# Optimization experiments

Hardware: AMD Instinct MI355X
Metric: run time of the kernel (lower is better)

## Reference

```python
import jax, jax.numpy as jnp
import numpy as np

N = 10000    # nodes in batched graph
E = 160000   # edges (avg degree 16)
G = 64       # graphs in batch
F_IN = 128
H = 256      # hidden width (forced equal everywhere by fc_1(1024,..) and readout sums)
HEADS = 2


def setup_inputs() -> dict:
    ks = jax.random.split(jax.random.key(0), 24)
    def w(k, shape, fan_in):
        return jax.random.normal(k, shape, dtype=jnp.float32) * np.float32(1.0 / np.sqrt(fan_in))
    return {
        "h": jax.random.normal(ks[0], (N, F_IN), dtype=jnp.float32),
        "src": jax.random.randint(ks[1], (E,), 0, N, dtype=jnp.int32),
        "dst": jax.random.randint(ks[2], (E,), 0, N, dtype=jnp.int32),
        # sorted graph ids, every graph guaranteed non-empty (avoids -inf from MaxPooling)
        "graph_ids": ((jnp.arange(N) * G) // N).astype(jnp.int32),
        "gcn1_W": w(ks[3], (F_IN, H), F_IN), "gcn1_b": jnp.zeros((H,), jnp.float32),
        "gcn2_W": w(ks[4], (H, H), H),       "gcn2_b": jnp.zeros((H,), jnp.float32),
        "gcn3_W": w(ks[5], (H, H), H),       "gcn3_b": jnp.zeros((H,), jnp.float32),
        "gat1_W": w(ks[6], (F_IN, HEADS * H), F_IN),
        "gat1_al": w(ks[7], (HEADS, H), H), "gat1_ar": w(ks[8], (HEADS, H), H),
        "gat1_b": jnp.zeros((HEADS * H,), jnp.float32),
        "gat2_W": w(ks[9], (H, HEADS * H), H),
        "gat2_al": w(ks[10], (HEADS, H), H), "gat2_ar": w(ks[11], (HEADS, H), H),
        "gat2_b": jnp.zeros((HEADS * H,), jnp.float32),
        "gat3_W": w(ks[12], (H, HEADS * H), H),
        "gat3_al": w(ks[13], (HEADS, H), H), "gat3_ar": w(ks[14], (HEADS, H), H),
        "gat3_b": jnp.zeros((HEADS * H,), jnp.float32),
        "fc1_W": w(ks[15], (4 * H, 128), 4 * H), "fc1_b": jnp.zeros((128,), jnp.float32),
        "fc2_W": w(ks[16], (128, 2), 128),       "fc2_b": jnp.zeros((2,), jnp.float32),
    }


def _forward(h, src, dst, graph_ids,
             gcn1_W, gcn1_b, gcn2_W, gcn2_b, gcn3_W, gcn3_b,
             gat1_W, gat1_al, gat1_ar, gat1_b,
             gat2_W, gat2_al, gat2_ar, gat2_b,
             gat3_W, gat3_al, gat3_ar, gat3_b,
             fc1_W, fc1_b, fc2_W, fc2_b):
    ones_e = jnp.ones((E,), jnp.float32)
    # DGL GraphConv norm='both': D_out^{-1/2} on src side, D_in^{-1/2} on dst side (deg clamped to 1)
    d_src = jnp.clip(jax.ops.segment_sum(ones_e, src, num_segments=N), 1.0) ** -0.5
    d_dst = jnp.clip(jax.ops.segment_sum(ones_e, dst, num_segments=N), 1.0) ** -0.5
    counts = jnp.clip(jax.ops.segment_sum(jnp.ones((N,), jnp.float32), graph_ids, num_segments=G), 1.0)

    def gcn(x, W, b):
        agg = jax.ops.segment_sum((x * d_src[:, None])[src], dst, num_segments=N) * d_dst[:, None]
        return jax.nn.relu(agg @ W + b)

    def gat(x, W, al, ar, b):
        z = (x @ W).reshape(N, HEADS, H)                 # [N, heads, H]
        e = jax.nn.leaky_relu(jnp.sum(z * al, -1)[src] + jnp.sum(z * ar, -1)[dst], 0.2)  # [E, heads]
        ex = jnp.exp(e - jax.ops.segment_max(e, dst, num_segments=N)[dst])
        alpha = ex / jax.ops.segment_sum(ex, dst, num_segments=N)[dst]  # edge softmax per dst
        o = jax.ops.segment_sum(alpha[:, :, None] * z[src], dst, num_segments=N)  # [N, heads, H]
        return jax.nn.relu(o + b.reshape(1, HEADS, H)).mean(axis=1)     # mean over heads, as in source

    def avgp(x):
        return jax.ops.segment_sum(x, graph_ids, num_segments=G) / counts[:, None]
    def maxp(x):
        return jax.ops.segment_max(x, graph_ids, num_segments=G)
    def readout(x):
        return jnp.concatenate([avgp(x), maxp(x)], axis=1)

    gcn1 = gcn(h, gcn1_W, gcn1_b);   r1 = readout(gcn1)
    gcn2 = gcn(gcn1, gcn2_W, gcn2_b); r2 = readout(gcn2)
    gcn3 = gcn(gcn2, gcn3_W, gcn3_b); r3 = readout(gcn3)
    g1 = gat(h, gat1_W, gat1_al, gat1_ar, gat1_b)   # spat_read_out1 computed but unused (faithful)
    g2 = gat(g1, gat2_W, gat2_al, gat2_ar, gat2_b); s2 = readout(g2)
    g3 = gat(g2, gat3_W, gat3_al, gat3_ar, gat3_b)
    s3 = jnp.concatenate([avgp(g2), maxp(g3)], axis=1)  # source: avg(gat2), max(gat3)

    spec = r1 + r2 + r3
    spat = r1 + s2 + s3  # source bug preserved: spat_merged starts from spec_read_out1
    merged = jnp.concatenate([spec, spat], axis=1)       # [G, 1024]
    f1 = jax.nn.relu(merged @ fc1_W + fc1_b)             # dropout p=0.0 -> identity
    return jax.nn.sigmoid(f1 @ fc2_W + fc2_b)            # [G, 2]


def reference(h, src, dst, graph_ids,
              gcn1_W, gcn1_b, gcn2_W, gcn2_b, gcn3_W, gcn3_b,
              gat1_W, gat1_al, gat1_ar, gat1_b,
              gat2_W, gat2_al, gat2_ar, gat2_b,
              gat3_W, gat3_al, gat3_ar, gat3_b,
              fc1_W, fc1_b, fc2_W, fc2_b):
    return _forward(h, src, dst, graph_ids,
                    gcn1_W, gcn1_b, gcn2_W, gcn2_b, gcn3_W, gcn3_b,
                    gat1_W, gat1_al, gat1_ar, gat1_b,
                    gat2_W, gat2_al, gat2_ar, gat2_b,
                    gat3_W, gat3_al, gat3_ar, gat3_b,
                    fc1_W, fc1_b, fc2_W, fc2_b)
```

## Files before the change

kernel.cpp:

```cpp
#include <hip/hip_runtime.h>
#include <math.h>

#define NN 10000
#define EE 160000
#define GG 64
#define FIN 128
#define HH 256
#define ZW 512
#define RS 8

typedef unsigned short u16;
using bf16x8 = __attribute__((ext_vector_type(8))) short;
using f32x4 = __attribute__((ext_vector_type(4))) float;

__device__ inline u16 f2bf(float x) {
  union { float f; unsigned u; } v; v.f = x;
  unsigned r = v.u + 0x7FFF + ((v.u >> 16) & 1);
  return (u16)(r >> 16);
}
__device__ inline float bf2f(u16 x) {
  union { unsigned u; float f; } v; v.u = ((unsigned)x) << 16; return v.f;
}
__device__ inline float bflo(unsigned pair) {
  union { unsigned u; float f; } v; v.u = pair << 16; return v.f;
}
__device__ inline float bfhi(unsigned pair) {
  union { unsigned u; float f; } v; v.u = pair & 0xFFFF0000u; return v.f;
}


__global__ __launch_bounds__(256) void k_count_prep(
    const int* __restrict__ src, const int* __restrict__ dst, int* deg_src, int* deg_dst,
    const float* __restrict__ gcn1_W, u16* __restrict__ gcn1_Wt,
    const float* __restrict__ gcn2_W, u16* __restrict__ gcn2_Wt,
    const float* __restrict__ gcn3_W, u16* __restrict__ gcn3_Wt,
    const float* __restrict__ gat1_W, u16* __restrict__ gat1_Wt,
    const float* __restrict__ gat2_W, u16* __restrict__ gat2_Wt,
    const float* __restrict__ gat3_W, u16* __restrict__ gat3_Wt,
    const float* __restrict__ h, u16* __restrict__ h_bf,
    const float* __restrict__ al1, const float* __restrict__ ar1,
    const float* __restrict__ al2, const float* __restrict__ ar2,
    const float* __restrict__ al3, const float* __restrict__ ar3,
    float* __restrict__ wl1, float* __restrict__ wr1,
    float* __restrict__ wl2, float* __restrict__ wr2,
    float* __restrict__ wl3, float* __restrict__ wr3) {
  int bb = blockIdx.x, t = threadIdx.x;
  if (bb < 625) {
    int e = bb * 256 + t;
    if (e < EE) {
      atomicAdd(&deg_src[src[e]], 1);
      atomicAdd(&deg_dst[dst[e]], 1);
    }
    return;
  }
  int b = bb - 625;
  if (b < 1920) {
    const float* W; u16* Wt; int K, N, idx;
    if (b < 128)       { W = gcn1_W; Wt = gcn1_Wt; K = 128; N = 256; idx = b * 256 + t; }
    else if (b < 384)  { W = gcn2_W; Wt = gcn2_Wt; K = 256; N = 256; idx = (b - 128) * 256 + t; }
    else if (b < 640)  { W = gcn3_W; Wt = gcn3_Wt; K = 256; N = 256; idx = (b - 384) * 256 + t; }
    else if (b < 896)  { W = gat1_W; Wt = gat1_Wt; K = 128; N = 512; idx = (b - 640) * 256 + t; }
    else if (b < 1408) { W = gat2_W; Wt = gat2_Wt; K = 256; N = 512; idx = (b - 896) * 256 + t; }
    else               { W = gat3_W; Wt = gat3_Wt; K = 256; N = 512; idx = (b - 1408) * 256 + t; }
    int k = idx / N, n = idx - k * N;
    Wt[(size_t)n * K + k] = f2bf(W[idx]);
  } else if (b < 3170) {
    int idx = (b - 1920) * 256 + t;
    float4 v = *(const float4*)&h[(size_t)idx * 4];
    ushort4 o;
    o.x = f2bf(v.x); o.y = f2bf(v.y); o.z = f2bf(v.z); o.w = f2bf(v.w);
    *(ushort4*)&h_bf[(size_t)idx * 4] = o;
  } else {
    int jb = b - 3170;
    const float* W; const float* al; const float* ar; float* wl; float* wr; int K, i;
    if (jb == 0)      { W = gat1_W; al = al1; ar = ar1; wl = wl1; wr = wr1; K = 128; i = t; }
    else if (jb <= 2) { W = gat2_W; al = al2; ar = ar2; wl = wl2; wr = wr2; K = 256; i = (jb - 1) * 256 + t; }
    else              { W = gat3_W; al = al3; ar = ar3; wl = wl3; wr = wr3; K = 256; i = (jb - 3) * 256 + t; }
    int hh = i / K, k = i - hh * K;
    float sl = 0.f, sr = 0.f;
    for (int f = 0; f < HH; f++) {
      float wv = W[(size_t)k * ZW + hh * HH + f];
      sl += wv * al[hh * HH + f];
      sr += wv * ar[hh * HH + f];
    }
    wl[hh * K + k] = sl;
    wr[hh * K + k] = sr;
  }
}

__global__ __launch_bounds__(1024) void k_norms_scan(
    const int* __restrict__ deg_src, const int* __restrict__ deg_dst,
    const int* __restrict__ gid, float* dsrc, float* ddst, int* gstart, int* row_ptr) {
  if (blockIdx.x < 10) {
    int n = blockIdx.x * 1024 + threadIdx.x;
    if (n < NN) {
      int a = deg_src[n]; if (a < 1) a = 1;
      int b = deg_dst[n]; if (b < 1) b = 1;
      dsrc[n] = 1.0f / sqrtf((float)a);
      ddst[n] = 1.0f / sqrtf((float)b);
      if (n == 0) gstart[gid[0]] = 0;
      else if (gid[n] != gid[n - 1]) gstart[gid[n]] = n;
      if (n == NN - 1) gstart[GG] = NN;
    }
    return;
  }
  __shared__ int wsum[16];
  __shared__ int carry;
  int lane = threadIdx.x & 63, wid = threadIdx.x >> 6;
  if (threadIdx.x == 0) { carry = 0; row_ptr[0] = 0; }
  __syncthreads();
  for (int base = 0; base < NN; base += 1024) {
    int i = base + threadIdx.x;
    int x = (i < NN) ? deg_dst[i] : 0;
#pragma unroll
    for (int off = 1; off < 64; off <<= 1) {
      int t = __shfl_up(x, off);
      if (lane >= off) x += t;
    }
    if (lane == 63) wsum[wid] = x;
    __syncthreads();
    if (wid == 0 && lane < 16) {
      int y = wsum[lane];
#pragma unroll
      for (int off = 1; off < 16; off <<= 1) {
        int t = __shfl_up(y, off, 16);
        if (lane >= off) y += t;
      }
      wsum[lane] = y;
    }
    __syncthreads();
    int woff = (wid > 0) ? wsum[wid - 1] : 0;
    if (i < NN) row_ptr[i + 1] = carry + woff + x;
    int total = wsum[15];
    __syncthreads();
    if (threadIdx.x == 0) carry += total;
    __syncthreads();
  }
}

__global__ void fill_csr_kernel(const int* __restrict__ src, const int* __restrict__ dst,
                                const int* __restrict__ row_ptr, int* fill, int* csr_src) {
  int e = blockIdx.x * blockDim.x + threadIdx.x;
  if (e < EE) {
    int d = dst[e];
    int p = atomicAdd(&fill[d], 1);
    csr_src[row_ptr[d] + p] = src[e];
  }
}

__global__ __launch_bounds__(64) void sort_rows_kernel(const int* __restrict__ row_ptr,
                                                       int* csr_src) {
  int n = blockIdx.x;
  int s0 = row_ptr[n];
  int L = row_ptr[n + 1] - s0;
  if (L <= 1) return;
  __shared__ int buf[512];
  if (L <= 512) {
    for (int i = threadIdx.x; i < L; i += 64) buf[i] = csr_src[s0 + i];
    __syncthreads();
    for (int i = threadIdx.x; i < L; i += 64) {
      int v = buf[i], r = 0;
      for (int j = 0; j < L; j++) {
        int u = buf[j];
        r += (u < v) || (u == v && j < i);
      }
      csr_src[s0 + r] = v;
    }
  } else if (threadIdx.x == 0) {
    for (int i = s0 + 1; i < s0 + L; i++) {
      int v = csr_src[i], j = i - 1;
      while (j >= s0 && csr_src[j] > v) { csr_src[j + 1] = csr_src[j]; j--; }
      csr_src[j + 1] = v;
    }
  }
}


__device__ inline void dev_gcn_agg(int n, int lane,
    const u16* __restrict__ xb, const float* __restrict__ dsrc, const float* __restrict__ ddst,
    const int* __restrict__ row_ptr, const int* __restrict__ csr_src,
    u16* __restrict__ out, int F) {
  int s0 = row_ptr[n], s1 = row_ptr[n + 1];
  float dd = ddst[n];
  if (F == 256) {
    int bf = lane * 4;
    float a0 = 0, a1 = 0, a2 = 0, a3 = 0;
    int e = s0;
    for (; e + 1 < s1; e += 2) {
      int sA = csr_src[e], sB = csr_src[e + 1];
      float wA = dsrc[sA], wB = dsrc[sB];
      uint2 vA = *(const uint2*)&xb[(size_t)sA * 256 + bf];
      uint2 vB = *(const uint2*)&xb[(size_t)sB * 256 + bf];
      a0 += wA * bflo(vA.x) + wB * bflo(vB.x);
      a1 += wA * bfhi(vA.x) + wB * bfhi(vB.x);
      a2 += wA * bflo(vA.y) + wB * bflo(vB.y);
      a3 += wA * bfhi(vA.y) + wB * bfhi(vB.y);
    }
    if (e < s1) {
      int s = csr_src[e];
      float w = dsrc[s];
      uint2 v = *(const uint2*)&xb[(size_t)s * 256 + bf];
      a0 += w * bflo(v.x); a1 += w * bfhi(v.x);
      a2 += w * bflo(v.y); a3 += w * bfhi(v.y);
    }
    ushort4 o;
    o.x = f2bf(a0 * dd); o.y = f2bf(a1 * dd); o.z = f2bf(a2 * dd); o.w = f2bf(a3 * dd);
    *(ushort4*)&out[(size_t)n * 256 + bf] = o;
  } else {
    int bf = lane * 2;
    float a0 = 0, a1 = 0;
    int e = s0;
    for (; e + 1 < s1; e += 2) {
      int sA = csr_src[e], sB = csr_src[e + 1];
      float wA = dsrc[sA], wB = dsrc[sB];
      unsigned vA = *(const unsigned*)&xb[(size_t)sA * 128 + bf];
      unsigned vB = *(const unsigned*)&xb[(size_t)sB * 128 + bf];
      a0 += wA * bflo(vA) + wB * bflo(vB);
      a1 += wA * bfhi(vA) + wB * bfhi(vB);
    }
    if (e < s1) {
      int s = csr_src[e];
      float w = dsrc[s];
      unsigned v = *(const unsigned*)&xb[(size_t)s * 128 + bf];
      a0 += w * bflo(v); a1 += w * bfhi(v);
    }
    ushort2 o;
    o.x = f2bf(a0 * dd); o.y = f2bf(a1 * dd);
    *(ushort2*)&out[(size_t)n * 128 + bf] = o;
  }
}

__device__ inline void dev_scores(int n, int lane, const float* __restrict__ x,
                                  const float* __restrict__ wl, const float* __restrict__ wr,
                                  float* __restrict__ asrc, float* __restrict__ adst, int K) {
  float a0 = 0, a1 = 0, b0 = 0, b1 = 0;
  for (int k = lane; k < K; k += 64) {
    float xv = x[(size_t)n * K + k];
    a0 += xv * wl[k];
    a1 += xv * wl[K + k];
    b0 += xv * wr[k];
    b1 += xv * wr[K + k];
  }
#pragma unroll
  for (int off = 32; off; off >>= 1) {
    a0 += __shfl_down(a0, off);
    a1 += __shfl_down(a1, off);
    b0 += __shfl_down(b0, off);
    b1 += __shfl_down(b1, off);
  }
  if (lane == 0) {
    asrc[n * 2 + 0] = a0; asrc[n * 2 + 1] = a1;
    adst[n * 2 + 0] = b0; adst[n * 2 + 1] = b1;
  }
}

__device__ inline void dev_alpha(int n, int lane,
    const float* __restrict__ asrc, const float* __restrict__ adst,
    const int* __restrict__ row_ptr, const int* __restrict__ csr_src,
    float* __restrict__ alpha) {
  int s0 = row_ptr[n], s1 = row_ptr[n + 1];
  if (s1 <= s0) return;
  float2 an = *(const float2*)&adst[n * 2];
  float m0 = -INFINITY, m1 = -INFINITY;
  for (int e = s0 + lane; e < s1; e += 64) {
    float2 as = *(const float2*)&asrc[csr_src[e] * 2];
    float e0 = as.x + an.x; e0 = (e0 > 0.f) ? e0 : 0.2f * e0;
    float e1 = as.y + an.y; e1 = (e1 > 0.f) ? e1 : 0.2f * e1;
    m0 = fmaxf(m0, e0); m1 = fmaxf(m1, e1);
  }
#pragma unroll
  for (int off = 32; off; off >>= 1) {
    m0 = fmaxf(m0, __shfl_xor(m0, off));
    m1 = fmaxf(m1, __shfl_xor(m1, off));
  }
  float s0f = 0.f, s1f = 0.f;
  for (int e = s0 + lane; e < s1; e += 64) {
    float2 as = *(const float2*)&asrc[csr_src[e] * 2];
    float e0 = as.x + an.x; e0 = (e0 > 0.f) ? e0 : 0.2f * e0;
    float e1 = as.y + an.y; e1 = (e1 > 0.f) ? e1 : 0.2f * e1;
    s0f += __expf(e0 - m0); s1f += __expf(e1 - m1);
  }
#pragma unroll
  for (int off = 32; off; off >>= 1) {
    s0f += __shfl_xor(s0f, off);
    s1f += __shfl_xor(s1f, off);
  }
  float i0 = (s0f > 0.f) ? 1.f / s0f : 0.f;
  float i1 = (s1f > 0.f) ? 1.f / s1f : 0.f;
  for (int e = s0 + lane; e < s1; e += 64) {
    float2 as = *(const float2*)&asrc[csr_src[e] * 2];
    float e0 = as.x + an.x; e0 = (e0 > 0.f) ? e0 : 0.2f * e0;
    float e1 = as.y + an.y; e1 = (e1 > 0.f) ? e1 : 0.2f * e1;
    float2 o; o.x = __expf(e0 - m0) * i0; o.y = __expf(e1 - m1) * i1;
    *(float2*)&alpha[e * 2] = o;
  }
}

#define BM 128
#define BN 64
#define BK 64
#define LPAD 8

__device__ inline void dev_gemm(const u16* __restrict__ A, const u16* __restrict__ Wt,
                                const float* __restrict__ bias, u16* __restrict__ Cb,
                                int K, int Nc, int relu, int bx, int by, int tid,
                                u16 (*As)[BK + LPAD], u16 (*Bs)[BK + LPAD]) {
  int lane = tid & 63;
  int wid = tid >> 6;
  int wm = wid & 1, wn = wid >> 1;
  int l15 = lane & 15, lg = lane >> 4;
  int row0 = bx * BM;
  int col0 = by * BN;
  f32x4 acc[4][2] = {};
  for (int k0 = 0; k0 < K; k0 += BK) {
#pragma unroll
    for (int p = 0; p < 4; p++) {
      int c = p * 256 + tid;
      int r = c >> 3, k8 = c & 7;
      uint4 v = make_uint4(0, 0, 0, 0);
      int gr = row0 + r;
      if (gr < NN) v = *(const uint4*)&A[(size_t)gr * K + k0 + k8 * 8];
      *(uint4*)&As[r][k8 * 8] = v;
    }
#pragma unroll
    for (int p = 0; p < 2; p++) {
      int c = p * 256 + tid;
      int r = c >> 3, k8 = c & 7;
      uint4 v = *(const uint4*)&Wt[(size_t)(col0 + r) * K + k0 + k8 * 8];
      *(uint4*)&Bs[r][k8 * 8] = v;
    }
    __syncthreads();
#pragma unroll
    for (int ks = 0; ks < BK; ks += 32) {
      bf16x8 afr[4], bfr[2];
#pragma unroll
      for (int m = 0; m < 4; m++)
        afr[m] = *(const bf16x8*)&As[wm * 64 + m * 16 + l15][ks + lg * 8];
#pragma unroll
      for (int n = 0; n < 2; n++)
        bfr[n] = *(const bf16x8*)&Bs[wn * 32 + n * 16 + l15][ks + lg * 8];
#pragma unroll
      for (int m = 0; m < 4; m++)
#pragma unroll
        for (int n = 0; n < 2; n++)
          acc[m][n] = __builtin_amdgcn_mfma_f32_16x16x32_bf16(afr[m], bfr[n], acc[m][n], 0, 0, 0);
    }
    __syncthreads();
  }
#pragma unroll
  for (int m = 0; m < 4; m++) {
#pragma unroll
    for (int n = 0; n < 2; n++) {
      int gc = col0 + wn * 32 + n * 16 + l15;
      float bv = bias ? bias[gc] : 0.f;
#pragma unroll
      for (int j = 0; j < 4; j++) {
        int gr = row0 + wm * 64 + m * 16 + lg * 4 + j;
        if (gr < NN) {
          float v = acc[m][n][j] + bv;
          if (relu) v = fmaxf(v, 0.f);
          Cb[(size_t)gr * Nc + gc] = f2bf(v);
        }
      }
    }
  }
}

__device__ inline void dev_gat_agg(int n, int tid,
    const u16* __restrict__ zb, const float* __restrict__ alpha, const float* __restrict__ b,
    const int* __restrict__ row_ptr, const int* __restrict__ csr_src,
    u16* __restrict__ out_bf,
    const float* __restrict__ wlN, const float* __restrict__ wrN,
    float* __restrict__ asrcN, float* __restrict__ adstN,
    float (*hv)[HH], float (*red)[4]) {
  int h = tid >> 7;
  int p = tid & 127;
  int s0 = row_ptr[n], s1 = row_ptr[n + 1];
  float a0 = 0.f, a1 = 0.f;
  int e = s0;
  for (; e + 1 < s1; e += 2) {
    int sA = csr_src[e], sB = csr_src[e + 1];
    float wA = alpha[e * 2 + h], wB = alpha[(e + 1) * 2 + h];
    unsigned zA = *(const unsigned*)&zb[(size_t)sA * ZW + h * HH + p * 2];
    unsigned zB = *(const unsigned*)&zb[(size_t)sB * ZW + h * HH + p * 2];
    a0 += wA * bflo(zA) + wB * bflo(zB);
    a1 += wA * bfhi(zA) + wB * bfhi(zB);
  }
  if (e < s1) {
    int s = csr_src[e];
    float w = alpha[e * 2 + h];
    unsigned zv = *(const unsigned*)&zb[(size_t)s * ZW + h * HH + p * 2];
    a0 += w * bflo(zv);
    a1 += w * bfhi(zv);
  }
  float r0 = fmaxf(a0 + b[h * HH + p * 2 + 0], 0.f);
  float r1 = fmaxf(a1 + b[h * HH + p * 2 + 1], 0.f);
  hv[h][p * 2 + 0] = r0;
  hv[h][p * 2 + 1] = r1;
  __syncthreads();
  float o = 0.5f * (hv[0][tid] + hv[1][tid]);
  out_bf[(size_t)n * HH + tid] = f2bf(o);
  if (wlN) {
    float p0 = o * wlN[tid], p1 = o * wlN[256 + tid];
    float q0 = o * wrN[tid], q1 = o * wrN[256 + tid];
    int lane = tid & 63, wid = tid >> 6;
#pragma unroll
    for (int off = 32; off; off >>= 1) {
      p0 += __shfl_down(p0, off);
      p1 += __shfl_down(p1, off);
      q0 += __shfl_down(q0, off);
      q1 += __shfl_down(q1, off);
    }
    if (lane == 0) { red[wid][0] = p0; red[wid][1] = p1; red[wid][2] = q0; red[wid][3] = q1; }
    __syncthreads();
    if (tid == 0) {
      asrcN[n * 2 + 0] = red[0][0] + red[1][0] + red[2][0] + red[3][0];
      asrcN[n * 2 + 1] = red[0][1] + red[1][1] + red[2][1] + red[3][1];
      adstN[n * 2 + 0] = red[0][2] + red[1][2] + red[2][2] + red[3][2];
      adstN[n * 2 + 1] = red[0][3] + red[1][3] + red[2][3] + red[3][3];
    }
  }
}

__device__ inline void dev_stage1(const u16* __restrict__ x, int l, int g, int s, int f,
                                  const int* __restrict__ gstart, float* __restrict__ partial) {
  int n0 = gstart[g], n1 = gstart[g + 1];
  int cnt = n1 - n0;
  int chunk = (cnt + RS - 1) / RS;
  int a = n0 + s * chunk;
  int bnd = a + chunk; if (bnd > n1) bnd = n1;
  float sum = 0.f, mx = -INFINITY;
  for (int n = a; n < bnd; n++) {
    float v = bf2f(x[(size_t)n * HH + f]);
    sum += v;
    mx = fmaxf(mx, v);
  }
  size_t base = ((size_t)l * GG * RS + g * RS + s) * 2 * HH;
  partial[base + f] = sum;
  partial[base + HH + f] = mx;
}

__device__ inline void dev_stage2(const float* __restrict__ partial, int l, int g, int t,
                                  const int* __restrict__ gstart, float* __restrict__ rr) {
  int f = t & 255, ismax = t >> 8;
  size_t base = ((size_t)l * GG * RS + g * RS) * 2 * HH;
  if (!ismax) {
    float s = 0.f;
    for (int k = 0; k < RS; k++) s += partial[base + (size_t)k * 2 * HH + f];
    rr[(size_t)l * GG * 512 + g * 512 + f] = s / (float)(gstart[g + 1] - gstart[g]);
  } else {
    float m = -INFINITY;
    for (int k = 0; k < RS; k++) m = fmaxf(m, partial[base + (size_t)k * 2 * HH + HH + f]);
    rr[(size_t)l * GG * 512 + g * 512 + 256 + f] = m;
  }
}


__global__ __launch_bounds__(256) void k_s1(
    const u16* __restrict__ h_bf, const float* __restrict__ h,
    const float* __restrict__ dsrc, const float* __restrict__ ddst,
    const int* __restrict__ row_ptr, const int* __restrict__ csr_src,
    u16* __restrict__ zagg, const float* __restrict__ wl1, const float* __restrict__ wr1,
    float* __restrict__ asrc, float* __restrict__ adst) {
  int b = blockIdx.x, t = threadIdx.x;
  int wid = t >> 6, lane = t & 63;
  if (b < 2500) {
    int n = b * 4 + wid;
    if (n < NN) dev_gcn_agg(n, lane, h_bf, dsrc, ddst, row_ptr, csr_src, zagg, FIN);
  } else {
    int n = (b - 2500) * 4 + wid;
    if (n < NN) dev_scores(n, lane, h, wl1, wr1, asrc, adst, FIN);
  }
}

__global__ __launch_bounds__(256) void k_gemms(
    const u16* __restrict__ A1, const u16* __restrict__ Wt1, const float* __restrict__ bias1,
    u16* __restrict__ C1, int K1,
    const u16* __restrict__ A2, const u16* __restrict__ Wt2, u16* __restrict__ C2, int K2,
    const float* __restrict__ asrc, const float* __restrict__ adst,
    const int* __restrict__ row_ptr, const int* __restrict__ csr_src,
    float* __restrict__ alpha) {
  __shared__ u16 As[BM][BK + LPAD];
  __shared__ u16 Bs[BN][BK + LPAD];
  int b = blockIdx.x, t = threadIdx.x;
  if (b < 316) {
    dev_gemm(A1, Wt1, bias1, C1, K1, HH, 1, b % 79, b / 79, t, As, Bs);
  } else if (b < 948) {
    int i = b - 316;
    dev_gemm(A2, Wt2, nullptr, C2, K2, ZW, 0, i % 79, i / 79, t, As, Bs);
  } else {
    int n = (b - 948) * 4 + (t >> 6);
    if (n < NN) dev_alpha(n, t & 63, asrc, adst, row_ptr, csr_src, alpha);
  }
}

__global__ __launch_bounds__(256) void k_s3(
    const u16* __restrict__ zb, const float* __restrict__ alpha, const float* __restrict__ gb,
    const int* __restrict__ row_ptr, const int* __restrict__ csr_src,
    u16* __restrict__ out_bf,
    const float* __restrict__ wlN, const float* __restrict__ wrN,
    float* __restrict__ asrcN, float* __restrict__ adstN,
    const u16* __restrict__ xb, const float* __restrict__ dsrc, const float* __restrict__ ddst,
    u16* __restrict__ zagg) {
  __shared__ float hv[2][HH];
  __shared__ float red[4][4];
  int b = blockIdx.x, t = threadIdx.x;
  if (b < 10000) {
    dev_gat_agg(b, t, zb, alpha, gb, row_ptr, csr_src, out_bf, wlN, wrN, asrcN, adstN, hv, red);
  } else {
    int n = (b - 10000) * 4 + (t >> 6);
    if (n < NN) dev_gcn_agg(n, t & 63, xb, dsrc, ddst, row_ptr, csr_src, zagg, HH);
  }
}

struct Acts4 { const u16* a[4]; };
__global__ __launch_bounds__(256) void k_s7(
    const u16* __restrict__ zb, const float* __restrict__ alpha, const float* __restrict__ gb,
    const int* __restrict__ row_ptr, const int* __restrict__ csr_src,
    u16* __restrict__ out_bf,
    Acts4 acts, const int* __restrict__ gstart, float* __restrict__ partial) {
  __shared__ float hv[2][HH];
  __shared__ float red[4][4];
  int b = blockIdx.x, t = threadIdx.x;
  if (b < 10000) {
    dev_gat_agg(b, t, zb, alpha, gb, row_ptr, csr_src, out_bf,
                nullptr, nullptr, nullptr, nullptr, hv, red);
  } else {
    int i = b - 10000;
    int l = i >> 9, rem = i & 511;
    dev_stage1(acts.a[l], l, rem >> 3, rem & 7, t, gstart, partial);
  }
}

__global__ __launch_bounds__(512) void k_s8(
    const u16* __restrict__ gb3, const int* __restrict__ gstart,
    float* __restrict__ partial, float* __restrict__ rr) {
  int b = blockIdx.x, t = threadIdx.x;
  if (b < 512) {
    if (t < 256) dev_stage1(gb3, 4, b >> 3, b & 7, t, gstart, partial);
  } else {
    int j = b - 512;
    dev_stage2(partial, j >> 6, j & 63, t, gstart, rr);
  }
}

__global__ __launch_bounds__(512) void k_s9(
    const float* __restrict__ partial, const int* __restrict__ gstart, float* __restrict__ rr) {
  dev_stage2(partial, 4, blockIdx.x, threadIdx.x, gstart, rr);
}

__global__ __launch_bounds__(128) void fc_head_kernel(
    const float* __restrict__ rr, const float* __restrict__ W1, const float* __restrict__ b1,
    const float* __restrict__ W2, const float* __restrict__ b2, float* __restrict__ out) {
  int g = blockIdx.x;
  int t = threadIdx.x;
  __shared__ float row[1024];
  __shared__ float f1[128];
  const float* R0 = rr + 0 * GG * 512 + g * 512;
  const float* R1 = rr + 1 * GG * 512 + g * 512;
  const float* R2 = rr + 2 * GG * 512 + g * 512;
  const float* R3 = rr + 3 * GG * 512 + g * 512;
  const float* R4 = rr + 4 * GG * 512 + g * 512;
  for (int c = t; c < 512; c += 128) {
    float spec = R0[c] + R1[c] + R2[c];
    float s3 = (c < 256) ? R3[c] : R4[c];
    float spat = R0[c] + R3[c] + s3;
    row[c] = spec;
    row[512 + c] = spat;
  }
  __syncthreads();
  float acc = b1[t];
  for (int k = 0; k < 1024; k++) acc += row[k] * W1[k * 128 + t];
  f1[t] = fmaxf(acc, 0.f);
  __syncthreads();
  if (t < 2) {
    float a = b2[t];
    for (int k = 0; k < 128; k++) a += f1[k] * W2[k * 2 + t];
    out[g * 2 + t] = 1.f / (1.f + expf(-a));
  }
}

extern "C" void kernel_launch(void* const* d_in, const int* in_sizes, int n_in,
                              void* d_out, int out_size, void* d_ws, size_t ws_size,
                              hipStream_t stream) {
  const float* h      = (const float*)d_in[0];
  const int*   src    = (const int*)d_in[1];
  const int*   dst    = (const int*)d_in[2];
  const int*   gid    = (const int*)d_in[3];
  const float* gcn1_W = (const float*)d_in[4];  const float* gcn1_b = (const float*)d_in[5];
  const float* gcn2_W = (const float*)d_in[6];  const float* gcn2_b = (const float*)d_in[7];
  const float* gcn3_W = (const float*)d_in[8];  const float* gcn3_b = (const float*)d_in[9];
  const float* gat1_W = (const float*)d_in[10]; const float* gat1_al = (const float*)d_in[11];
  const float* gat1_ar= (const float*)d_in[12]; const float* gat1_b = (const float*)d_in[13];
  const float* gat2_W = (const float*)d_in[14]; const float* gat2_al = (const float*)d_in[15];
  const float* gat2_ar= (const float*)d_in[16]; const float* gat2_b = (const float*)d_in[17];
  const float* gat3_W = (const float*)d_in[18]; const float* gat3_al = (const float*)d_in[19];
  const float* gat3_ar= (const float*)d_in[20]; const float* gat3_b = (const float*)d_in[21];
  const float* fc1_W  = (const float*)d_in[22]; const float* fc1_b = (const float*)d_in[23];
  const float* fc2_W  = (const float*)d_in[24]; const float* fc2_b = (const float*)d_in[25];

  char* ws = (char*)d_ws;
  size_t off = 0;
  auto alloc = [&](size_t bytes) -> void* {
    void* p = ws + off;
    off += (bytes + 255) & ~(size_t)255;
    return p;
  };
  u16*   Zb      = (u16*)alloc((size_t)NN * ZW * 2);
  u16*   Zagg_bf = (u16*)alloc((size_t)NN * HH * 2);
  u16*   h_bf    = (u16*)alloc((size_t)NN * FIN * 2);
  u16*   ab1     = (u16*)alloc((size_t)NN * HH * 2);
  u16*   ab2     = (u16*)alloc((size_t)NN * HH * 2);
  u16*   ab3     = (u16*)alloc((size_t)NN * HH * 2);
  u16*   gb1     = (u16*)alloc((size_t)NN * HH * 2);
  u16*   gb2     = (u16*)alloc((size_t)NN * HH * 2);
  u16*   gb3     = (u16*)alloc((size_t)NN * HH * 2);
  int*   row_ptr = (int*)alloc((NN + 1) * 4);
  int*   csr_src = (int*)alloc((size_t)EE * 4);
  int*   meta    = (int*)alloc((size_t)3 * NN * 4);
  int*   deg_src = meta;
  int*   deg_dst = meta + NN;
  int*   fill    = meta + 2 * NN;
  float* dsrc    = (float*)alloc(NN * 4);
  float* ddst    = (float*)alloc(NN * 4);
  int*   gstart  = (int*)alloc((GG + 1) * 4);
  float* asrc    = (float*)alloc(NN * 2 * 4);
  float* adst    = (float*)alloc(NN * 2 * 4);
  float* alpha   = (float*)alloc((size_t)EE * 2 * 4);
  float* wl1     = (float*)alloc(2 * FIN * 4);
  float* wr1     = (float*)alloc(2 * FIN * 4);
  float* wl2     = (float*)alloc(2 * HH * 4);
  float* wr2     = (float*)alloc(2 * HH * 4);
  float* wl3     = (float*)alloc(2 * HH * 4);
  float* wr3     = (float*)alloc(2 * HH * 4);
  float* partial = (float*)alloc((size_t)5 * GG * RS * 2 * HH * 4);
  float* rr      = (float*)alloc((size_t)5 * GG * 512 * 4);
  u16* gcn1_Wt = (u16*)alloc((size_t)FIN * HH * 2);
  u16* gcn2_Wt = (u16*)alloc((size_t)HH * HH * 2);
  u16* gcn3_Wt = (u16*)alloc((size_t)HH * HH * 2);
  u16* gat1_Wt = (u16*)alloc((size_t)FIN * ZW * 2);
  u16* gat2_Wt = (u16*)alloc((size_t)HH * ZW * 2);
  u16* gat3_Wt = (u16*)alloc((size_t)HH * ZW * 2);

  hipMemsetAsync(meta, 0, (size_t)3 * NN * 4, stream);
  k_count_prep<<<3800, 256, 0, stream>>>(
      src, dst, deg_src, deg_dst,
      gcn1_W, gcn1_Wt, gcn2_W, gcn2_Wt, gcn3_W, gcn3_Wt,
      gat1_W, gat1_Wt, gat2_W, gat2_Wt, gat3_W, gat3_Wt,
      h, h_bf,
      gat1_al, gat1_ar, gat2_al, gat2_ar, gat3_al, gat3_ar,
      wl1, wr1, wl2, wr2, wl3, wr3);
  k_norms_scan<<<11, 1024, 0, stream>>>(deg_src, deg_dst, gid, dsrc, ddst, gstart, row_ptr);
  fill_csr_kernel<<<625, 256, 0, stream>>>(src, dst, row_ptr, fill, csr_src);
  sort_rows_kernel<<<NN, 64, 0, stream>>>(row_ptr, csr_src);

  k_s1<<<5000, 256, 0, stream>>>(h_bf, h, dsrc, ddst, row_ptr, csr_src, Zagg_bf,
                                 wl1, wr1, asrc, adst);
  k_gemms<<<3448, 256, 0, stream>>>(Zagg_bf, gcn1_Wt, gcn1_b, ab1, FIN,
                                    h_bf, gat1_Wt, Zb, FIN,
                                    asrc, adst, row_ptr, csr_src, alpha);
  k_s3<<<12500, 256, 0, stream>>>(Zb, alpha, gat1_b, row_ptr, csr_src, gb1,
                                  wl2, wr2, asrc, adst,
                                  ab1, dsrc, ddst, Zagg_bf);
  k_gemms<<<3448, 256, 0, stream>>>(Zagg_bf, gcn2_Wt, gcn2_b, ab2, HH,
                                    gb1, gat2_Wt, Zb, HH,
                                    asrc, adst, row_ptr, csr_src, alpha);
  k_s3<<<12500, 256, 0, stream>>>(Zb, alpha, gat2_b, row_ptr, csr_src, gb2,
                                  wl3, wr3, asrc, adst,
                                  ab2, dsrc, ddst, Zagg_bf);
  k_gemms<<<3448, 256, 0, stream>>>(Zagg_bf, gcn3_Wt, gcn3_b, ab3, HH,
                                    gb2, gat3_Wt, Zb, HH,
                                    asrc, adst, row_ptr, csr_src, alpha);
  Acts4 acts;
  acts.a[0] = ab1; acts.a[1] = ab2; acts.a[2] = ab3; acts.a[3] = gb2;
  k_s7<<<12048, 256, 0, stream>>>(Zb, alpha, gat3_b, row_ptr, csr_src, gb3,
                                  acts, gstart, partial);
  k_s8<<<768, 512, 0, stream>>>(gb3, gstart, partial, rr);
  k_s9<<<GG, 512, 0, stream>>>(partial, gstart, rr);
  fc_head_kernel<<<GG, 128, 0, stream>>>(rr, fc1_W, fc1_b, fc2_W, fc2_b, (float*)d_out);
}
```

Before: 295.9 us.

## Aggregate GAT features before projection and restructure kernel pipeline

GAT layers now compute attention scores from per-layer projected vectors on the input features, then aggregate the raw input features per head (F wide) before running the projection GEMM on the aggregated result. This reorders the computation to aggregate-then-transform, removing the materialized alpha buffer and shrinking the gathered row width from 512 to F per head. It also fuses the head-mean, bias and ReLU into the GEMM epilogue, and reshuffles readout stages across kernels. In exchange the GEMM input becomes NN x 2F, and oversized-degree rows fall back to recomputing the attention weights.

```diff
diff --git a/kernel.cpp b/kernel.cpp
--- a/kernel.cpp
+++ b/kernel.cpp
@@ -27,6 +27,15 @@
 __device__ inline float bfhi(unsigned pair) {
   union { unsigned u; float f; } v; v.u = pair & 0xFFFF0000u; return v.f;
 }
+
+#define BM 128
+#define BN 64
+#define BK 64
+#define LPAD 8
+
+struct SmemGemm { u16 As[BM][BK + LPAD]; u16 Bs[BN][BK + LPAD]; };
+struct SmemGatGemm { u16 A[2][64][BK + LPAD]; u16 B[2][64][BK + LPAD]; };
+struct SmemFuse { float al[2][512]; int idx[512]; float inv[2]; float mm[2]; };
 
 
 __global__ __launch_bounds__(256) void k_count_prep(
@@ -138,16 +147,6 @@
   }
 }
 
-__global__ void fill_csr_kernel(const int* __restrict__ src, const int* __restrict__ dst,
-                                const int* __restrict__ row_ptr, int* fill, int* csr_src) {
-  int e = blockIdx.x * blockDim.x + threadIdx.x;
-  if (e < EE) {
-    int d = dst[e];
-    int p = atomicAdd(&fill[d], 1);
-    csr_src[row_ptr[d] + p] = src[e];
-  }
-}
-
 __global__ __launch_bounds__(64) void sort_rows_kernel(const int* __restrict__ row_ptr,
                                                        int* csr_src) {
   int n = blockIdx.x;
@@ -254,57 +253,151 @@
   }
 }
 
-__device__ inline void dev_alpha(int n, int lane,
+__device__ inline void dev_scores_bf(int n, int lane, const u16* __restrict__ xb,
+                                     const float* __restrict__ wl, const float* __restrict__ wr,
+                                     float* __restrict__ asrc, float* __restrict__ adst) {
+  float a0 = 0, a1 = 0, b0 = 0, b1 = 0;
+#pragma unroll
+  for (int idx = lane; idx < 128; idx += 64) {
+    unsigned v = *(const unsigned*)&xb[(size_t)n * 256 + idx * 2];
+    float lo = bflo(v), hi = bfhi(v);
+    a0 += lo * wl[idx * 2] + hi * wl[idx * 2 + 1];
+    a1 += lo * wl[256 + idx * 2] + hi * wl[256 + idx * 2 + 1];
+    b0 += lo * wr[idx * 2] + hi * wr[idx * 2 + 1];
+    b1 += lo * wr[256 + idx * 2] + hi * wr[256 + idx * 2 + 1];
+  }
+#pragma unroll
+  for (int off = 32; off; off >>= 1) {
+    a0 += __shfl_down(a0, off);
+    a1 += __shfl_down(a1, off);
+    b0 += __shfl_down(b0, off);
+    b1 += __shfl_down(b1, off);
+  }
+  if (lane == 0) {
+    asrc[n * 2 + 0] = a0; asrc[n * 2 + 1] = a1;
+    adst[n * 2 + 0] = b0; adst[n * 2 + 1] = b1;
+  }
+}
+
+__device__ inline void dev_gatfuse(int n, int tid,
+    const u16* __restrict__ xb, int F,
     const float* __restrict__ asrc, const float* __restrict__ adst,
     const int* __restrict__ row_ptr, const int* __restrict__ csr_src,
-    float* __restrict__ alpha) {
-  int s0 = row_ptr[n], s1 = row_ptr[n + 1];
-  if (s1 <= s0) return;
+    u16* __restrict__ gx, SmemFuse& sf) {
+  int lane = tid & 63;
+  int s0 = row_ptr[n];
+  int deg = row_ptr[n + 1] - s0;
   float2 an = *(const float2*)&adst[n * 2];
-  float m0 = -INFINITY, m1 = -INFINITY;
-  for (int e = s0 + lane; e < s1; e += 64) {
-    float2 as = *(const float2*)&asrc[csr_src[e] * 2];
-    float e0 = as.x + an.x; e0 = (e0 > 0.f) ? e0 : 0.2f * e0;
-    float e1 = as.y + an.y; e1 = (e1 > 0.f) ? e1 : 0.2f * e1;
-    m0 = fmaxf(m0, e0); m1 = fmaxf(m1, e1);
-  }
-#pragma unroll
-  for (int off = 32; off; off >>= 1) {
-    m0 = fmaxf(m0, __shfl_xor(m0, off));
-    m1 = fmaxf(m1, __shfl_xor(m1, off));
-  }
-  float s0f = 0.f, s1f = 0.f;
-  for (int e = s0 + lane; e < s1; e += 64) {
-    float2 as = *(const float2*)&asrc[csr_src[e] * 2];
-    float e0 = as.x + an.x; e0 = (e0 > 0.f) ? e0 : 0.2f * e0;
-    float e1 = as.y + an.y; e1 = (e1 > 0.f) ? e1 : 0.2f * e1;
-    s0f += __expf(e0 - m0); s1f += __expf(e1 - m1);
-  }
-#pragma unroll
-  for (int off = 32; off; off >>= 1) {
-    s0f += __shfl_xor(s0f, off);
-    s1f += __shfl_xor(s1f, off);
-  }
-  float i0 = (s0f > 0.f) ? 1.f / s0f : 0.f;
-  float i1 = (s1f > 0.f) ? 1.f / s1f : 0.f;
-  for (int e = s0 + lane; e < s1; e += 64) {
-    float2 as = *(const float2*)&asrc[csr_src[e] * 2];
-    float e0 = as.x + an.x; e0 = (e0 > 0.f) ? e0 : 0.2f * e0;
-    float e1 = as.y + an.y; e1 = (e1 > 0.f) ? e1 : 0.2f * e1;
-    float2 o; o.x = __expf(e0 - m0) * i0; o.y = __expf(e1 - m1) * i1;
-    *(float2*)&alpha[e * 2] = o;
-  }
-}
-
-#define BM 128
-#define BN 64
-#define BK 64
-#define LPAD 8
+  if (tid < 64) {
+    if (deg <= 512) {
+      float m0 = -INFINITY, m1 = -INFINITY;
+      for (int i = lane; i < deg; i += 64) {
+        int s = csr_src[s0 + i];
+        sf.idx[i] = s;
+        float2 as = *(const float2*)&asrc[s * 2];
+        float e0 = as.x + an.x; e0 = (e0 > 0.f) ? e0 : 0.2f * e0;
+        float e1 = as.y + an.y; e1 = (e1 > 0.f) ? e1 : 0.2f * e1;
+        sf.al[0][i] = e0; sf.al[1][i] = e1;
+        m0 = fmaxf(m0, e0); m1 = fmaxf(m1, e1);
+      }
+#pragma unroll
+      for (int off = 32; off; off >>= 1) {
+        m0 = fmaxf(m0, __shfl_xor(m0, off));
+        m1 = fmaxf(m1, __shfl_xor(m1, off));
+      }
+      float t0 = 0.f, t1 = 0.f;
+      for (int i = lane; i < deg; i += 64) {
+        float w0 = __expf(sf.al[0][i] - m0);
+        float w1 = __expf(sf.al[1][i] - m1);
+        sf.al[0][i] = w0; sf.al[1][i] = w1;
+        t0 += w0; t1 += w1;
+      }
+#pragma unroll
+      for (int off = 32; off; off >>= 1) {
+        t0 += __shfl_xor(t0, off);
+        t1 += __shfl_xor(t1, off);
+      }
+      if (lane == 0) {
+        sf.inv[0] = (t0 > 0.f) ? 1.f / t0 : 0.f;
+        sf.inv[1] = (t1 > 0.f) ? 1.f / t1 : 0.f;
+      }
+    } else {
+      float m0 = -INFINITY, m1 = -INFINITY;
+      for (int i = lane; i < deg; i += 64) {
+        float2 as = *(const float2*)&asrc[csr_src[s0 + i] * 2];
+        float e0 = as.x + an.x; e0 = (e0 > 0.f) ? e0 : 0.2f * e0;
+        float e1 = as.y + an.y; e1 = (e1 > 0.f) ? e1 : 0.2f * e1;
+        m0 = fmaxf(m0, e0); m1 = fmaxf(m1, e1);
+      }
+#pragma unroll
+      for (int off = 32; off; off >>= 1) {
+        m0 = fmaxf(m0, __shfl_xor(m0, off));
+        m1 = fmaxf(m1, __shfl_xor(m1, off));
+      }
+      float t0 = 0.f, t1 = 0.f;
+      for (int i = lane; i < deg; i += 64) {
+        float2 as = *(const float2*)&asrc[csr_src[s0 + i] * 2];
+        float e0 = as.x + an.x; e0 = (e0 > 0.f) ? e0 : 0.2f * e0;
+        float e1 = as.y + an.y; e1 = (e1 > 0.f) ? e1 : 0.2f * e1;
+        t0 += __expf(e0 - m0); t1 += __expf(e1 - m1);
+      }
+#pragma unroll
+      for (int off = 32; off; off >>= 1) {
+        t0 += __shfl_xor(t0, off);
+        t1 += __shfl_xor(t1, off);
+      }
+      if (lane == 0) {
+        sf.inv[0] = (t0 > 0.f) ? 1.f / t0 : 0.f;
+        sf.inv[1] = (t1 > 0.f) ? 1.f / t1 : 0.f;
+        sf.mm[0] = m0; sf.mm[1] = m1;
+      }
+    }
+  }
+  __syncthreads();
+  int hthr = (F == 256) ? 256 : 128;
+  if (tid >= hthr) return;
+  int hshift = (F == 256) ? 7 : 6;
+  int h = tid >> hshift;
+  int p = tid & ((F >> 1) - 1);
+  float inv = sf.inv[h];
+  float a0 = 0.f, a1 = 0.f;
+  if (deg <= 512) {
+    int i = 0;
+    for (; i + 1 < deg; i += 2) {
+      int sA = sf.idx[i], sB = sf.idx[i + 1];
+      float wA = sf.al[h][i] * inv, wB = sf.al[h][i + 1] * inv;
+      unsigned vA = *(const unsigned*)&xb[(size_t)sA * F + p * 2];
+      unsigned vB = *(const unsigned*)&xb[(size_t)sB * F + p * 2];
+      a0 += wA * bflo(vA) + wB * bflo(vB);
+      a1 += wA * bfhi(vA) + wB * bfhi(vB);
+    }
+    if (i < deg) {
+      int s = sf.idx[i];
+      float w = sf.al[h][i] * inv;
+      unsigned v = *(const unsigned*)&xb[(size_t)s * F + p * 2];
+      a0 += w * bflo(v); a1 += w * bfhi(v);
+    }
+  } else {
+    float anh = (h == 0) ? an.x : an.y;
+    float mh = sf.mm[h];
+    for (int i = 0; i < deg; i++) {
+      int s = csr_src[s0 + i];
+      float e = asrc[s * 2 + h] + anh;
+      e = (e > 0.f) ? e : 0.2f * e;
+      float w = __expf(e - mh) * inv;
+      unsigned v = *(const unsigned*)&xb[(size_t)s * F + p * 2];
+      a0 += w * bflo(v); a1 += w * bfhi(v);
+    }
+  }
+  ushort2 o;
+  o.x = f2bf(a0); o.y = f2bf(a1);
+  *(ushort2*)&gx[(size_t)n * (2 * F) + h * F + p * 2] = o;
+}
 
 __device__ inline void dev_gemm(const u16* __restrict__ A, const u16* __restrict__ Wt,
                                 const float* __restrict__ bias, u16* __restrict__ Cb,
                                 int K, int Nc, int relu, int bx, int by, int tid,
-                                u16 (*As)[BK + LPAD], u16 (*Bs)[BK + LPAD]) {
+                                SmemGemm& sm) {
   int lane = tid & 63;
   int wid = tid >> 6;
   int wm = wid & 1, wn = wid >> 1;
@@ -320,14 +413,14 @@
       uint4 v = make_uint4(0, 0, 0, 0);
       int gr = row0 + r;
       if (gr < NN) v = *(const uint4*)&A[(size_t)gr * K + k0 + k8 * 8];
-      *(uint4*)&As[r][k8 * 8] = v;
+      *(uint4*)&sm.As[r][k8 * 8] = v;
     }
 #pragma unroll
     for (int p = 0; p < 2; p++) {
       int c = p * 256 + tid;
       int r = c >> 3, k8 = c & 7;
       uint4 v = *(const uint4*)&Wt[(size_t)(col0 + r) * K + k0 + k8 * 8];
-      *(uint4*)&Bs[r][k8 * 8] = v;
+      *(uint4*)&sm.Bs[r][k8 * 8] = v;
     }
     __syncthreads();
 #pragma unroll
@@ -335,29 +428,29 @@
       bf16x8 afr[4], bfr[2];
 #pragma unroll
       for (int m = 0; m < 4; m++)
-        afr[m] = *(const bf16x8*)&As[wm * 64 + m * 16 + l15][ks + lg * 8];
-#pragma unroll
-      for (int n = 0; n < 2; n++)
-        bfr[n] = *(const bf16x8*)&Bs[wn * 32 + n * 16 + l15][ks + lg * 8];
+        afr[m] = *(const bf16x8*)&sm.As[wm * 64 + m * 16 + l15][ks + lg * 8];
+#pragma unroll
+      for (int nn = 0; nn < 2; nn++)
+        bfr[nn] = *(const bf16x8*)&sm.Bs[wn * 32 + nn * 16 + l15][ks + lg * 8];
 #pragma unroll
       for (int m = 0; m < 4; m++)
 #pragma unroll
-        for (int n = 0; n < 2; n++)
-          acc[m][n] = __builtin_amdgcn_mfma_f32_16x16x32_bf16(afr[m], bfr[n], acc[m][n], 0, 0, 0);
+        for (int nn = 0; nn < 2; nn++)
+          acc[m][nn] = __builtin_amdgcn_mfma_f32_16x16x32_bf16(afr[m], bfr[nn], acc[m][nn], 0, 0, 0);
     }
     __syncthreads();
   }
 #pragma unroll
   for (int m = 0; m < 4; m++) {
 #pragma unroll
-    for (int n = 0; n < 2; n++) {
-      int gc = col0 + wn * 32 + n * 16 + l15;
+    for (int nn = 0; nn < 2; nn++) {
+      int gc = col0 + wn * 32 + nn * 16 + l15;
       float bv = bias ? bias[gc] : 0.f;
 #pragma unroll
       for (int j = 0; j < 4; j++) {
         int gr = row0 + wm * 64 + m * 16 + lg * 4 + j;
         if (gr < NN) {
-          float v = acc[m][n][j] + bv;
+          float v = acc[m][nn][j] + bv;
           if (relu) v = fmaxf(v, 0.f);
           Cb[(size_t)gr * Nc + gc] = f2bf(v);
         }
@@ -366,58 +459,75 @@
   }
 }
 
-__device__ inline void dev_gat_agg(int n, int tid,
-    const u16* __restrict__ zb, const float* __restrict__ alpha, const float* __restrict__ b,
-    const int* __restrict__ row_ptr, const int* __restrict__ csr_src,
-    u16* __restrict__ out_bf,
-    const float* __restrict__ wlN, const float* __restrict__ wrN,
-    float* __restrict__ asrcN, float* __restrict__ adstN,
-    float (*hv)[HH], float (*red)[4]) {
-  int h = tid >> 7;
-  int p = tid & 127;
-  int s0 = row_ptr[n], s1 = row_ptr[n + 1];
-  float a0 = 0.f, a1 = 0.f;
-  int e = s0;
-  for (; e + 1 < s1; e += 2) {
-    int sA = csr_src[e], sB = csr_src[e + 1];
-    float wA = alpha[e * 2 + h], wB = alpha[(e + 1) * 2 + h];
-    unsigned zA = *(const unsigned*)&zb[(size_t)sA * ZW + h * HH + p * 2];
-    unsigned zB = *(const unsigned*)&zb[(size_t)sB * ZW + h * HH + p * 2];
-    a0 += wA * bflo(zA) + wB * bflo(zB);
-    a1 += wA * bfhi(zA) + wB * bfhi(zB);
-  }
-  if (e < s1) {
-    int s = csr_src[e];
-    float w = alpha[e * 2 + h];
-    unsigned zv = *(const unsigned*)&zb[(size_t)s * ZW + h * HH + p * 2];
-    a0 += w * bflo(zv);
-    a1 += w * bfhi(zv);
-  }
-  float r0 = fmaxf(a0 + b[h * HH + p * 2 + 0], 0.f);
-  float r1 = fmaxf(a1 + b[h * HH + p * 2 + 1], 0.f);
-  hv[h][p * 2 + 0] = r0;
-  hv[h][p * 2 + 1] = r1;
-  __syncthreads();
-  float o = 0.5f * (hv[0][tid] + hv[1][tid]);
-  out_bf[(size_t)n * HH + tid] = f2bf(o);
-  if (wlN) {
-    float p0 = o * wlN[tid], p1 = o * wlN[256 + tid];
-    float q0 = o * wrN[tid], q1 = o * wrN[256 + tid];
-    int lane = tid & 63, wid = tid >> 6;
-#pragma unroll
-    for (int off = 32; off; off >>= 1) {
-      p0 += __shfl_down(p0, off);
-      p1 += __shfl_down(p1, off);
-      q0 += __shfl_down(q0, off);
-      q1 += __shfl_down(q1, off);
-    }
-    if (lane == 0) { red[wid][0] = p0; red[wid][1] = p1; red[wid][2] = q0; red[wid][3] = q1; }
+__device__ inline void dev_gat_gemm(const u16* __restrict__ gx, const u16* __restrict__ Wt,
+                                    const float* __restrict__ bias, u16* __restrict__ gb,
+                                    int K, int bx, int by, int tid, SmemGatGemm& sm) {
+  int lane = tid & 63;
+  int wid = tid >> 6;
+  int wm = wid & 1, wn = wid >> 1;
+  int l15 = lane & 15, lg = lane >> 4;
+  int row0 = bx * 64;
+  int col0 = by * 64;
+  int str = 2 * K;
+  f32x4 acc[2][2][2] = {};
+  for (int k0 = 0; k0 < K; k0 += BK) {
+#pragma unroll
+    for (int hh = 0; hh < 2; hh++) {
+#pragma unroll
+      for (int p = 0; p < 2; p++) {
+        int c = p * 256 + tid;
+        int r = c >> 3, k8 = c & 7;
+        int gr = row0 + r;
+        uint4 v = make_uint4(0, 0, 0, 0);
+        if (gr < NN) v = *(const uint4*)&gx[(size_t)gr * str + hh * K + k0 + k8 * 8];
+        *(uint4*)&sm.A[hh][r][k8 * 8] = v;
+      }
+#pragma unroll
+      for (int p = 0; p < 2; p++) {
+        int c = p * 256 + tid;
+        int r = c >> 3, k8 = c & 7;
+        uint4 v = *(const uint4*)&Wt[(size_t)(hh * 256 + col0 + r) * K + k0 + k8 * 8];
+        *(uint4*)&sm.B[hh][r][k8 * 8] = v;
+      }
+    }
     __syncthreads();
-    if (tid == 0) {
-      asrcN[n * 2 + 0] = red[0][0] + red[1][0] + red[2][0] + red[3][0];
-      asrcN[n * 2 + 1] = red[0][1] + red[1][1] + red[2][1] + red[3][1];
-      adstN[n * 2 + 0] = red[0][2] + red[1][2] + red[2][2] + red[3][2];
-      adstN[n * 2 + 1] = red[0][3] + red[1][3] + red[2][3] + red[3][3];
+#pragma unroll
+    for (int ks = 0; ks < BK; ks += 32) {
+      bf16x8 af[2][2], bf_[2][2];
+#pragma unroll
+      for (int hh = 0; hh < 2; hh++) {
+#pragma unroll
+        for (int m = 0; m < 2; m++)
+          af[hh][m] = *(const bf16x8*)&sm.A[hh][wm * 32 + m * 16 + l15][ks + lg * 8];
+#pragma unroll
+        for (int nn = 0; nn < 2; nn++)
+          bf_[hh][nn] = *(const bf16x8*)&sm.B[hh][wn * 32 + nn * 16 + l15][ks + lg * 8];
+      }
+#pragma unroll
+      for (int hh = 0; hh < 2; hh++)
+#pragma unroll
+        for (int m = 0; m < 2; m++)
+#pragma unroll
+          for (int nn = 0; nn < 2; nn++)
+            acc[hh][m][nn] = __builtin_amdgcn_mfma_f32_16x16x32_bf16(af[hh][m], bf_[hh][nn], acc[hh][m][nn], 0, 0, 0);
+    }
+    __syncthreads();
+  }
+#pragma unroll
+  for (int m = 0; m < 2; m++) {
+#pragma unroll
+    for (int nn = 0; nn < 2; nn++) {
+      int gc = col0 + wn * 32 + nn * 16 + l15;
+      float bv0 = bias[gc], bv1 = bias[256 + gc];
+#pragma unroll
+      for (int j = 0; j < 4; j++) {
+        int gr = row0 + wm * 32 + m * 16 + lg * 4 + j;
+        if (gr < NN) {
+          float r0 = fmaxf(acc[0][m][nn][j] + bv0, 0.f);
+          float r1 = fmaxf(acc[1][m][nn][j] + bv1, 0.f);
+          gb[(size_t)gr * 256 + gc] = f2bf(0.5f * (r0 + r1));
+        }
+      }
     }
   }
 }
@@ -440,138 +550,204 @@
   partial[base + HH + f] = mx;
 }
 
-__device__ inline void dev_stage2(const float* __restrict__ partial, int l, int g, int t,
-                                  const int* __restrict__ gstart, float* __restrict__ rr) {
-  int f = t & 255, ismax = t >> 8;
+__device__ inline float dev_stage2_val(const float* __restrict__ partial, int l, int g, int tt,
+                                       const int* __restrict__ gstart) {
+  int f = tt & 255, ismax = tt >> 8;
   size_t base = ((size_t)l * GG * RS + g * RS) * 2 * HH;
   if (!ismax) {
     float s = 0.f;
     for (int k = 0; k < RS; k++) s += partial[base + (size_t)k * 2 * HH + f];
-    rr[(size_t)l * GG * 512 + g * 512 + f] = s / (float)(gstart[g + 1] - gstart[g]);
+    return s / (float)(gstart[g + 1] - gstart[g]);
   } else {
     float m = -INFINITY;
     for (int k = 0; k < RS; k++) m = fmaxf(m, partial[base + (size_t)k * 2 * HH + HH + f]);
-    rr[(size_t)l * GG * 512 + g * 512 + 256 + f] = m;
-  }
-}
-
-
-__global__ __launch_bounds__(256) void k_s1(
-    const u16* __restrict__ h_bf, const float* __restrict__ h,
-    const float* __restrict__ dsrc, const float* __restrict__ ddst,
-    const int* __restrict__ row_ptr, const int* __restrict__ csr_src,
-    u16* __restrict__ zagg, const float* __restrict__ wl1, const float* __restrict__ wr1,
+    return m;
+  }
+}
+
+
+__global__ __launch_bounds__(256) void k_fill_scores(
+    const int* __restrict__ src, const int* __restrict__ dst,
+    const int* __restrict__ row_ptr, int* fill, int* csr_src,
+    const float* __restrict__ h, const float* __restrict__ wl1, const float* __restrict__ wr1,
     float* __restrict__ asrc, float* __restrict__ adst) {
   int b = blockIdx.x, t = threadIdx.x;
-  int wid = t >> 6, lane = t & 63;
+  if (b < 625) {
+    int e = b * 256 + t;
+    if (e < EE) {
+      int d = dst[e];
+      int p = atomicAdd(&fill[d], 1);
+      csr_src[row_ptr[d] + p] = src[e];
+    }
+  } else {
+    int n = (b - 625) * 4 + (t >> 6);
+    if (n < NN) dev_scores(n, t & 63, h, wl1, wr1, asrc, adst, FIN);
+  }
+}
+
+__global__ __launch_bounds__(256) void k_s1(
+    const u16* __restrict__ h_bf, const float* __restrict__ dsrc, const float* __restrict__ ddst,
+    const int* __restrict__ row_ptr, const int* __restrict__ csr_src,
+    u16* __restrict__ zagg, const float* __restrict__ asrc, const float* __restrict__ adst,
+    u16* __restrict__ gx) {
+  __shared__ SmemFuse sf;
+  int b = blockIdx.x, t = threadIdx.x;
   if (b < 2500) {
-    int n = b * 4 + wid;
-    if (n < NN) dev_gcn_agg(n, lane, h_bf, dsrc, ddst, row_ptr, csr_src, zagg, FIN);
-  } else {
-    int n = (b - 2500) * 4 + wid;
-    if (n < NN) dev_scores(n, lane, h, wl1, wr1, asrc, adst, FIN);
-  }
-}
-
-__global__ __launch_bounds__(256) void k_gemms(
-    const u16* __restrict__ A1, const u16* __restrict__ Wt1, const float* __restrict__ bias1,
-    u16* __restrict__ C1, int K1,
-    const u16* __restrict__ A2, const u16* __restrict__ Wt2, u16* __restrict__ C2, int K2,
-    const float* __restrict__ asrc, const float* __restrict__ adst,
-    const int* __restrict__ row_ptr, const int* __restrict__ csr_src,
-    float* __restrict__ alpha) {
-  __shared__ u16 As[BM][BK + LPAD];
-  __shared__ u16 Bs[BN][BK + LPAD];
+    int n = b * 4 + (t >> 6);
+    if (n < NN) dev_gcn_agg(n, t & 63, h_bf, dsrc, ddst, row_ptr, csr_src, zagg, FIN);
+  } else {
+    dev_gatfuse(b - 2500, t, h_bf, FIN, asrc, adst, row_ptr, csr_src, gx, sf);
+  }
+}
+
+__global__ __launch_bounds__(256) void k_g1(
+    const u16* __restrict__ zagg, const u16* __restrict__ gcn1_Wt, const float* __restrict__ gcn1_b,
+    u16* __restrict__ ab1,
+    const u16* __restrict__ gx, const u16* __restrict__ gat1_Wt, const float* __restrict__ gat1_b,
+    u16* __restrict__ gb1) {
+  __shared__ union { SmemGemm g; SmemGatGemm gg; } sm;
   int b = blockIdx.x, t = threadIdx.x;
   if (b < 316) {
-    dev_gemm(A1, Wt1, bias1, C1, K1, HH, 1, b % 79, b / 79, t, As, Bs);
-  } else if (b < 948) {
+    dev_gemm(zagg, gcn1_Wt, gcn1_b, ab1, FIN, HH, 1, b % 79, b / 79, t, sm.g);
+  } else {
     int i = b - 316;
-    dev_gemm(A2, Wt2, nullptr, C2, K2, ZW, 0, i % 79, i / 79, t, As, Bs);
-  } else {
-    int n = (b - 948) * 4 + (t >> 6);
-    if (n < NN) dev_alpha(n, t & 63, asrc, adst, row_ptr, csr_src, alpha);
-  }
-}
-
-__global__ __launch_bounds__(256) void k_s3(
-    const u16* __restrict__ zb, const float* __restrict__ alpha, const float* __restrict__ gb,
-    const int* __restrict__ row_ptr, const int* __restrict__ csr_src,
-    u16* __restrict__ out_bf,
-    const float* __restrict__ wlN, const float* __restrict__ wrN,
-    float* __restrict__ asrcN, float* __restrict__ adstN,
-    const u16* __restrict__ xb, const float* __restrict__ dsrc, const float* __restrict__ ddst,
-    u16* __restrict__ zagg) {
-  __shared__ float hv[2][HH];
-  __shared__ float red[4][4];
+    dev_gat_gemm(gx, gat1_Wt, gat1_b, gb1, FIN, i / 4, i % 4, t, sm.gg);
+  }
+}
+
+__global__ __launch_bounds__(256) void k_s2(
+    const u16* __restrict__ ab_prev, const float* __restrict__ dsrc, const float* __restrict__ ddst,
+    const int* __restrict__ row_ptr, const int* __restrict__ csr_src, u16* __restrict__ zagg,
+    const u16* __restrict__ gb_prev, const float* __restrict__ wl, const float* __restrict__ wr,
+    float* __restrict__ asrc, float* __restrict__ adst) {
+  int b = blockIdx.x, t = threadIdx.x;
+  if (b < 2500) {
+    int n = b * 4 + (t >> 6);
+    if (n < NN) dev_gcn_agg(n, t & 63, ab_prev, dsrc, ddst, row_ptr, csr_src, zagg, HH);
+  } else {
+    int n = (b - 2500) * 4 + (t >> 6);
+    if (n < NN) dev_scores_bf(n, t & 63, gb_prev, wl, wr, asrc, adst);
+  }
+}
+
+__global__ __launch_bounds__(256) void k_g2(
+    const u16* __restrict__ zagg, const u16* __restrict__ gcn_Wt, const float* __restrict__ gcn_b,
+    u16* __restrict__ ab_out,
+    const u16* __restrict__ gb_prev, const float* __restrict__ asrc, const float* __restrict__ adst,
+    const int* __restrict__ row_ptr, const int* __restrict__ csr_src, u16* __restrict__ gx) {
+  __shared__ union { SmemGemm g; SmemFuse f; } sm;
+  int b = blockIdx.x, t = threadIdx.x;
+  if (b < 316) {
+    dev_gemm(zagg, gcn_Wt, gcn_b, ab_out, HH, HH, 1, b % 79, b / 79, t, sm.g);
+  } else {
+    dev_gatfuse(b - 316, t, gb_prev, HH, asrc, adst, row_ptr, csr_src, gx, sm.f);
+  }
+}
+
+__global__ __launch_bounds__(256) void k_s3n(
+    const u16* __restrict__ gx, const u16* __restrict__ gat_Wt, const float* __restrict__ gat_b,
+    u16* __restrict__ gb_out,
+    const u16* __restrict__ ab_prev, const float* __restrict__ dsrc, const float* __restrict__ ddst,
+    const int* __restrict__ row_ptr, const int* __restrict__ csr_src, u16* __restrict__ zagg) {
+  __shared__ SmemGatGemm sm;
+  int b = blockIdx.x, t = threadIdx.x;
+  if (b < 628) {
+    dev_gat_gemm(gx, gat_Wt, gat_b, gb_out, HH, b / 4, b % 4, t, sm);
+  } else {
+    int n = (b - 628) * 4 + (t >> 6);
+    if (n < NN) dev_gcn_agg(n, t & 63, ab_prev, dsrc, ddst, row_ptr, csr_src, zagg, HH);
+  }
+}
+
+struct Acts2 { const u16* a[2]; };
+__global__ __launch_bounds__(256) void k_g3(
+    const u16* __restrict__ zagg, const u16* __restrict__ gcn3_Wt, const float* __restrict__ gcn3_b,
+    u16* __restrict__ ab3,
+    const u16* __restrict__ gb2, const float* __restrict__ wl3, const float* __restrict__ wr3,
+    float* __restrict__ asrc, float* __restrict__ adst,
+    Acts2 acts, const int* __restrict__ gstart, float* __restrict__ partial) {
+  __shared__ SmemGemm sm;
+  int b = blockIdx.x, t = threadIdx.x;
+  if (b < 316) {
+    dev_gemm(zagg, gcn3_Wt, gcn3_b, ab3, HH, HH, 1, b % 79, b / 79, t, sm);
+  } else if (b < 2816) {
+    int n = (b - 316) * 4 + (t >> 6);
+    if (n < NN) dev_scores_bf(n, t & 63, gb2, wl3, wr3, asrc, adst);
+  } else {
+    int i = b - 2816;
+    int l = i >> 9, rem = i & 511;
+    dev_stage1(acts.a[l], l, rem >> 3, rem & 7, t, gstart, partial);
+  }
+}
+
+__global__ __launch_bounds__(256) void k_s4(
+    const u16* __restrict__ gb2, const float* __restrict__ asrc, const float* __restrict__ adst,
+    const int* __restrict__ row_ptr, const int* __restrict__ csr_src, u16* __restrict__ gx,
+    Acts2 acts, const int* __restrict__ gstart, float* __restrict__ partial) {
+  __shared__ SmemFuse sf;
   int b = blockIdx.x, t = threadIdx.x;
   if (b < 10000) {
-    dev_gat_agg(b, t, zb, alpha, gb, row_ptr, csr_src, out_bf, wlN, wrN, asrcN, adstN, hv, red);
-  } else {
-    int n = (b - 10000) * 4 + (t >> 6);
-    if (n < NN) dev_gcn_agg(n, t & 63, xb, dsrc, ddst, row_ptr, csr_src, zagg, HH);
-  }
-}
-
-struct Acts4 { const u16* a[4]; };
-__global__ __launch_bounds__(256) void k_s7(
-    const u16* __restrict__ zb, const float* __restrict__ alpha, const float* __restrict__ gb,
-    const int* __restrict__ row_ptr, const int* __restrict__ csr_src,
-    u16* __restrict__ out_bf,
-    Acts4 acts, const int* __restrict__ gstart, float* __restrict__ partial) {
-  __shared__ float hv[2][HH];
-  __shared__ float red[4][4];
-  int b = blockIdx.x, t = threadIdx.x;
-  if (b < 10000) {
-    dev_gat_agg(b, t, zb, alpha, gb, row_ptr, csr_src, out_bf,
-                nullptr, nullptr, nullptr, nullptr, hv, red);
+    dev_gatfuse(b, t, gb2, HH, asrc, adst, row_ptr, csr_src, gx, sf);
   } else {
     int i = b - 10000;
     int l = i >> 9, rem = i & 511;
-    dev_stage1(acts.a[l], l, rem >> 3, rem & 7, t, gstart, partial);
-  }
-}
-
-__global__ __launch_bounds__(512) void k_s8(
-    const u16* __restrict__ gb3, const int* __restrict__ gstart,
-    float* __restrict__ partial, float* __restrict__ rr) {
+    dev_stage1(acts.a[l], 2 + l, rem >> 3, rem & 7, t, gstart, partial);
+  }
+}
+
+__global__ __launch_bounds__(256) void k_g4(
+    const u16* __restrict__ gx, const u16* __restrict__ gat3_Wt, const float* __restrict__ gat3_b,
+    u16* __restrict__ gb3,
+    const float* __restrict__ partial, const int* __restrict__ gstart, float* __restrict__ rr) {
+  __shared__ SmemGatGemm sm;
   int b = blockIdx.x, t = threadIdx.x;
-  if (b < 512) {
-    if (t < 256) dev_stage1(gb3, 4, b >> 3, b & 7, t, gstart, partial);
-  } else {
-    int j = b - 512;
-    dev_stage2(partial, j >> 6, j & 63, t, gstart, rr);
-  }
-}
-
-__global__ __launch_bounds__(512) void k_s9(
-    const float* __restrict__ partial, const int* __restrict__ gstart, float* __restrict__ rr) {
-  dev_stage2(partial, 4, blockIdx.x, threadIdx.x, gstart, rr);
-}
-
-__global__ __launch_bounds__(128) void fc_head_kernel(
-    const float* __restrict__ rr, const float* __restrict__ W1, const float* __restrict__ b1,
+  if (b < 628) {
+    dev_gat_gemm(gx, gat3_Wt, gat3_b, gb3, HH, b / 4, b % 4, t, sm);
+  } else {
+    int i = b - 628;
+    int l = i >> 7, rem = i & 127;
+    int g = rem >> 1, half = rem & 1;
+    int tt = half * 256 + t;
+    rr[(size_t)l * GG * 512 + g * 512 + tt] = dev_stage2_val(partial, l, g, tt, gstart);
+  }
+}
+
+__global__ __launch_bounds__(256) void k_r1(
+    const u16* __restrict__ gb3, const int* __restrict__ gstart, float* __restrict__ partial) {
+  int b = blockIdx.x;
+  dev_stage1(gb3, 4, b >> 3, b & 7, threadIdx.x, gstart, partial);
+}
+
+__global__ __launch_bounds__(512) void k_fc(
+    const float* __restrict__ partial, const float* __restrict__ rr,
+    const int* __restrict__ gstart,
+    const float* __restrict__ W1, const float* __restrict__ b1,
     const float* __restrict__ W2, const float* __restrict__ b2, float* __restrict__ out) {
   int g = blockIdx.x;
   int t = threadIdx.x;
   __shared__ float row[1024];
   __shared__ float f1[128];
-  const float* R0 = rr + 0 * GG * 512 + g * 512;
-  const float* R1 = rr + 1 * GG * 512 + g * 512;
-  const float* R2 = rr + 2 * GG * 512 + g * 512;
-  const float* R3 = rr + 3 * GG * 512 + g * 512;
-  const float* R4 = rr + 4 * GG * 512 + g * 512;
-  for (int c = t; c < 512; c += 128) {
+  __shared__ float r4[512];
+  r4[t] = dev_stage2_val(partial, 4, g, t, gstart);
+  __syncthreads();
+  {
+    int c = t;
+    const float* R0 = rr + 0 * GG * 512 + g * 512;
+    const float* R1 = rr + 1 * GG * 512 + g * 512;
+    const float* R2 = rr + 2 * GG * 512 + g * 512;
+    const float* R3 = rr + 3 * GG * 512 + g * 512;
     float spec = R0[c] + R1[c] + R2[c];
-    float s3 = (c < 256) ? R3[c] : R4[c];
+    float s3 = (c < 256) ? R3[c] : r4[c];
     float spat = R0[c] + R3[c] + s3;
     row[c] = spec;
     row[512 + c] = spat;
   }
   __syncthreads();
-  float acc = b1[t];
-  for (int k = 0; k < 1024; k++) acc += row[k] * W1[k * 128 + t];
-  f1[t] = fmaxf(acc, 0.f);
+  if (t < 128) {
+    float acc = b1[t];
+    for (int k = 0; k < 1024; k++) acc += row[k] * W1[k * 128 + t];
+    f1[t] = fmaxf(acc, 0.f);
+  }
   __syncthreads();
   if (t < 2) {
     float a = b2[t];
@@ -606,8 +782,8 @@
     off += (bytes + 255) & ~(size_t)255;
     return p;
   };
-  u16*   Zb      = (u16*)alloc((size_t)NN * ZW * 2);
-  u16*   Zagg_bf = (u16*)alloc((size_t)NN * HH * 2);
+  u16*   gx      = (u16*)alloc((size_t)NN * ZW * 2);
+  u16*   Zagg    = (u16*)alloc((size_t)NN * HH * 2);
   u16*   h_bf    = (u16*)alloc((size_t)NN * FIN * 2);
   u16*   ab1     = (u16*)alloc((size_t)NN * HH * 2);
   u16*   ab2     = (u16*)alloc((size_t)NN * HH * 2);
@@ -626,7 +802,6 @@
   int*   gstart  = (int*)alloc((GG + 1) * 4);
   float* asrc    = (float*)alloc(NN * 2 * 4);
   float* adst    = (float*)alloc(NN * 2 * 4);
-  float* alpha   = (float*)alloc((size_t)EE * 2 * 4);
   float* wl1     = (float*)alloc(2 * FIN * 4);
   float* wr1     = (float*)alloc(2 * FIN * 4);
   float* wl2     = (float*)alloc(2 * HH * 4);
@@ -651,31 +826,26 @@
       gat1_al, gat1_ar, gat2_al, gat2_ar, gat3_al, gat3_ar,
       wl1, wr1, wl2, wr2, wl3, wr3);
   k_norms_scan<<<11, 1024, 0, stream>>>(deg_src, deg_dst, gid, dsrc, ddst, gstart, row_ptr);
-  fill_csr_kernel<<<625, 256, 0, stream>>>(src, dst, row_ptr, fill, csr_src);
+  k_fill_scores<<<3125, 256, 0, stream>>>(src, dst, row_ptr, fill, csr_src,
+                                          h, wl1, wr1, asrc, adst);
   sort_rows_kernel<<<NN, 64, 0, stream>>>(row_ptr, csr_src);
 
-  k_s1<<<5000, 256, 0, stream>>>(h_bf, h, dsrc, ddst, row_ptr, csr_src, Zagg_bf,
-                                 wl1, wr1, asrc, adst);
-  k_gemms<<<3448, 256, 0, stream>>>(Zagg_bf, gcn1_Wt, gcn1_b, ab1, FIN,
-                                    h_bf, gat1_Wt, Zb, FIN,
-                                    asrc, adst, row_ptr, csr_src, alpha);
-  k_s3<<<12500, 256, 0, stream>>>(Zb, alpha, gat1_b, row_ptr, csr_src, gb1,
-                                  wl2, wr2, asrc, adst,
-                                  ab1, dsrc, ddst, Zagg_bf);
-  k_gemms<<<3448, 256, 0, stream>>>(Zagg_bf, gcn2_Wt, gcn2_b, ab2, HH,
-                                    gb1, gat2_Wt, Zb, HH,
-                                    asrc, adst, row_ptr, csr_src, alpha);
-  k_s3<<<12500, 256, 0, stream>>>(Zb, alpha, gat2_b, row_ptr, csr_src, gb2,
-                                  wl3, wr3, asrc, adst,
-                                  ab2, dsrc, ddst, Zagg_bf);
-  k_gemms<<<3448, 256, 0, stream>>>(Zagg_bf, gcn3_Wt, gcn3_b, ab3, HH,
-                                    gb2, gat3_Wt, Zb, HH,
-                                    asrc, adst, row_ptr, csr_src, alpha);
-  Acts4 acts;
-  acts.a[0] = ab1; acts.a[1] = ab2; acts.a[2] = ab3; acts.a[3] = gb2;
-  k_s7<<<12048, 256, 0, stream>>>(Zb, alpha, gat3_b, row_ptr, csr_src, gb3,
-                                  acts, gstart, partial);
-  k_s8<<<768, 512, 0, stream>>>(gb3, gstart, partial, rr);
-  k_s9<<<GG, 512, 0, stream>>>(partial, gstart, rr);
-  fc_head_kernel<<<GG, 128, 0, stream>>>(rr, fc1_W, fc1_b, fc2_W, fc2_b, (float*)d_out);
-}
+  k_s1<<<12500, 256, 0, stream>>>(h_bf, dsrc, ddst, row_ptr, csr_src, Zagg, asrc, adst, gx);
+  k_g1<<<944, 256, 0, stream>>>(Zagg, gcn1_Wt, gcn1_b, ab1, gx, gat1_Wt, gat1_b, gb1);
+  k_s2<<<5000, 256, 0, stream>>>(ab1, dsrc, ddst, row_ptr, csr_src, Zagg,
+                                 gb1, wl2, wr2, asrc, adst);
+  k_g2<<<10316, 256, 0, stream>>>(Zagg, gcn2_Wt, gcn2_b, ab2,
+                                  gb1, asrc, adst, row_ptr, csr_src, gx);
+  k_s3n<<<3128, 256, 0, stream>>>(gx, gat2_Wt, gat2_b, gb2,
+                                  ab2, dsrc, ddst, row_ptr, csr_src, Zagg);
+  Acts2 a01; a01.a[0] = ab1; a01.a[1] = ab2;
+  k_g3<<<3840, 256, 0, stream>>>(Zagg, gcn3_Wt, gcn3_b, ab3,
+                                 gb2, wl3, wr3, asrc, adst,
+                                 a01, gstart, partial);
+  Acts2 a23; a23.a[0] = ab3; a23.a[1] = gb2;
+  k_s4<<<11024, 256, 0, stream>>>(gb2, asrc, adst, row_ptr, csr_src, gx,
+                                  a23, gstart, partial);
+  k_g4<<<1140, 256, 0, stream>>>(gx, gat3_Wt, gat3_b, gb3, partial, gstart, rr);
+  k_r1<<<512, 256, 0, stream>>>(gb3, gstart, partial);
+  k_fc<<<GG, 512, 0, stream>>>(partial, rr, gstart, fc1_W, fc1_b, fc2_W, fc2_b, (float*)d_out);
+}
```

Result: slower. 307.6 us (+3.9%).
